# Kernel tuning notes

Measured on AMD Instinct MI355X. Metric: run time of the kernel, lower is better.

## Reference

```python
import jax, jax.numpy as jnp
import numpy as np

NUM_GROUPS = 32
EPS = 1e-5
HT_MIN = -1.0
HT_MAX = 1.0


def setup_inputs() -> dict:
    key = jax.random.key(0)
    k1, k2, k3 = jax.random.split(key, 3)
    B, IN, OUT = 8192, 2048, 4096
    x = jax.random.normal(k1, (B, IN), dtype=jnp.float32)
    # kaiming-uniform-ish scale for weight, uniform bias in [-1/sqrt(fan_in), 1/sqrt(fan_in)]
    bound_w = np.sqrt(1.0 / IN)
    weight = jax.random.uniform(k2, (OUT, IN), dtype=jnp.float32, minval=-bound_w, maxval=bound_w)
    bias = jax.random.uniform(k3, (OUT,), dtype=jnp.float32, minval=-bound_w, maxval=bound_w)
    return {"x": x, "weight": weight, "bias": bias}


def reference(x, weight, bias):
    # GEMM + bias: (B, out)
    y = jnp.einsum('bi,oi->bo', x, weight) + bias
    B, OUT = y.shape
    fpg = OUT // NUM_GROUPS
    g = y.reshape(B, NUM_GROUPS, fpg)
    mean = jnp.mean(g, axis=-1, keepdims=True)
    var = jnp.mean(jnp.square(g - mean), axis=-1, keepdims=True)  # biased variance
    x_hat = (g - mean) / jnp.sqrt(var + EPS)
    out = jnp.clip(x_hat, HT_MIN, HT_MAX)
    return out.reshape(B, OUT)
```

## Files before the change

kernel.cpp:

```cpp
#include <hip/hip_runtime.h>
#include <hip/hip_bf16.h>

#define B_ROWS   8192
#define K_DIM    2048
#define OUT_COLS 4096
#define EPS      1e-5f

#define BM 256
#define BN 256
#define BK 64
#define NT (K_DIM / BK)

using f32x4  = __attribute__((ext_vector_type(4))) float;
using bf16x8 = __attribute__((ext_vector_type(8))) short;

__device__ __forceinline__ unsigned short f2bf_rn(float f) {
    unsigned u = __builtin_bit_cast(unsigned, f);
    u += 0x7FFFu + ((u >> 16) & 1u);
    return (unsigned short)(u >> 16);
}

__global__ void cvt_bf16(const float* __restrict__ in, unsigned short* __restrict__ out, int n4) {
    int stride = gridDim.x * blockDim.x;
    for (int i = blockIdx.x * blockDim.x + threadIdx.x; i < n4; i += stride) {
        float4 v = reinterpret_cast<const float4*>(in)[i];
        ushort4 r;
        r.x = f2bf_rn(v.x); r.y = f2bf_rn(v.y); r.z = f2bf_rn(v.z); r.w = f2bf_rn(v.w);
        reinterpret_cast<ushort4*>(out)[i] = r;
    }
}

__device__ __forceinline__ void gload16(const unsigned short* src, unsigned short* lds) {
    __builtin_amdgcn_global_load_lds((const __attribute__((address_space(1))) void*)src,
                                     (__attribute__((address_space(3))) void*)lds,
                                     16, 0, 0);
}

#define STA(BUF, H, KT) do {                                                        \
    gload16(Ag + (H)*262144 + (KT)*64 + goff0, &As[BUF][(H)*8192 + lds0]);          \
    gload16(Ag + (H)*262144 + (KT)*64 + goff1, &As[BUF][(H)*8192 + lds1]);          \
  } while (0)
#define STB(BUF, H, KT) do {                                                        \
    gload16(Bg + (H)*262144 + (KT)*64 + goff0, &Bs[BUF][(H)*8192 + lds0]);          \
    gload16(Bg + (H)*262144 + (KT)*64 + goff1, &Bs[BUF][(H)*8192 + lds1]);          \
  } while (0)

#define RD_B(CURB) do {                                                             \
    _Pragma("unroll") for (int n = 0; n < 4; ++n) {                                 \
      const int ro = browb + n * 16 * BK;                                           \
      bb[n][0] = *(const bf16x8*)&(CURB)[ro + colsw0];                              \
      bb[n][1] = *(const bf16x8*)&(CURB)[ro + colsw1];                              \
    } } while (0)

#define RD_A(SLOT, CURA, Q) do {                                                    \
    _Pragma("unroll") for (int dm = 0; dm < 2; ++dm) {                              \
      const int ro = arow + (2*(Q)+dm) * 16 * BK;                                   \
      af[SLOT][dm][0] = *(const bf16x8*)&(CURA)[ro + colsw0];                       \
      af[SLOT][dm][1] = *(const bf16x8*)&(CURA)[ro + colsw1];                       \
    } } while (0)

#define MFMA16(SLOT, Q) do {                                                        \
    __builtin_amdgcn_s_setprio(1);                                                  \
    _Pragma("unroll") for (int kk = 0; kk < 2; ++kk)                                \
      _Pragma("unroll") for (int dm = 0; dm < 2; ++dm)                              \
        _Pragma("unroll") for (int n = 0; n < 4; ++n)                               \
          acc[2*(Q)+dm][n] = __builtin_amdgcn_mfma_f32_16x16x32_bf16(               \
              af[SLOT][dm][kk], bb[n][kk], acc[2*(Q)+dm][n], 0, 0, 0);              \
    __builtin_amdgcn_s_setprio(0);                                                  \
  } while (0)

#define VW4  asm volatile("s_waitcnt vmcnt(4)" ::: "memory")
#define BAR  __builtin_amdgcn_s_barrier()

__global__ __launch_bounds__(512, 2) void gemm_gn(const unsigned short* __restrict__ A,
                                                  const unsigned short* __restrict__ Bw,
                                                  const float* __restrict__ bias,
                                                  float* __restrict__ out) {
    __shared__ __align__(16) unsigned short As[2][BM * BK];
    __shared__ __align__(16) unsigned short Bs[2][BN * BK];

    const int tid  = threadIdx.x;
    const int lane = tid & 63;
    const int wave = tid >> 6;
    const int wr   = wave >> 2;
    const int wcn  = wave & 3;
    const int l16  = lane & 15;
    const int lhi  = lane >> 4;

    const int bid  = blockIdx.x;
    const int swz  = (bid & 7) * (gridDim.x >> 3) + (bid >> 3);
    const int brow = swz >> 4;
    const int bcol = swz & 15;

    int goff0, goff1, lds0, lds1;
    {
        int f0 = tid;          int r0 = f0 >> 3;
        int f1 = 512 + tid;    int r1 = f1 >> 3;
        goff0 = r0 * K_DIM + (((f0 & 7) ^ (r0 & 7)) * 8);
        goff1 = r1 * K_DIM + (((f1 & 7) ^ (r1 & 7)) * 8);
        lds0  = f0 * 8;
        lds1  = f1 * 8;
    }
    const unsigned short* Ag = A  + (size_t)brow * BM * K_DIM;
    const unsigned short* Bg = Bw + (size_t)bcol * BN * K_DIM;

    const int colsw0 = (0 * 32 + lhi * 8) ^ ((l16 & 7) << 3);
    const int colsw1 = (1 * 32 + lhi * 8) ^ ((l16 & 7) << 3);
    const int arow   = (wr * 128 + l16) * BK;
    const int browb  = (wcn * 64 + l16) * BK;

    const unsigned short* A0p = &As[0][0];
    const unsigned short* A1p = &As[1][0];
    const unsigned short* B0p = &Bs[0][0];
    const unsigned short* B1p = &Bs[1][0];

    f32x4  acc[8][4] = {};
    bf16x8 af[2][2][2];
    bf16x8 bb[4][2];

    STA(0, 0, 0); STA(0, 1, 0);
    STB(0, 0, 0); STB(0, 1, 0);
    STB(1, 0, 1); STB(1, 1, 1);
    VW4;
    BAR;
    RD_A(0, A0p, 0);
    RD_B(B0p);

    #pragma unroll 1
    for (int tt = 0; tt < NT; tt += 2) {
        const int k1 = (tt + 1) & (NT - 1);
        const int k2 = (tt + 2) & (NT - 1);
        const int k3 = (tt + 3) & (NT - 1);
        RD_A(1, A0p, 1); STA(1, 0, k1);               MFMA16(0, 0);       BAR;
        RD_A(0, A0p, 2); STA(1, 1, k1); STB(0, 0, k2); MFMA16(1, 1);      BAR;
        RD_A(1, A0p, 3); STB(0, 1, k2);               MFMA16(0, 2); VW4;  BAR;
        RD_A(0, A1p, 0);                              MFMA16(1, 3); RD_B(B1p); BAR;
        RD_A(1, A1p, 1); STA(0, 0, k2);               MFMA16(0, 0);       BAR;
        RD_A(0, A1p, 2); STA(0, 1, k2); STB(1, 0, k3); MFMA16(1, 1);      BAR;
        RD_A(1, A1p, 3); STB(1, 1, k3);               MFMA16(0, 2); VW4;  BAR;
        RD_A(0, A0p, 0);                              MFMA16(1, 3); RD_B(B0p); BAR;
    }

    asm volatile("s_waitcnt vmcnt(0)" ::: "memory");
    __syncthreads();
    float* red = (float*)&As[0][0];

    float bv[4];
    #pragma unroll
    for (int n = 0; n < 4; ++n)
        bv[n] = bias[bcol * BN + wcn * 64 + n * 16 + l16];

    #pragma unroll
    for (int m = 0; m < 8; ++m) {
        #pragma unroll
        for (int j = 0; j < 4; ++j) {
            float s = 0.f, s2 = 0.f;
            #pragma unroll
            for (int n = 0; n < 4; ++n) {
                float v = acc[m][n][j] + bv[n];
                acc[m][n][j] = v;
                s += v; s2 += v * v;
            }
            #pragma unroll
            for (int o = 1; o < 16; o <<= 1) {
                s  += __shfl_xor(s,  o);
                s2 += __shfl_xor(s2, o);
            }
            if (l16 == 0) {
                int r = wr * 128 + m * 16 + lhi * 4 + j;
                red[r * 8 + wcn * 2 + 0] = s;
                red[r * 8 + wcn * 2 + 1] = s2;
            }
        }
    }
    __syncthreads();

    const int p2 = (wcn & 2) * 2;
    #pragma unroll
    for (int m = 0; m < 8; ++m) {
        #pragma unroll
        for (int j = 0; j < 4; ++j) {
            const int r   = wr * 128 + m * 16 + lhi * 4 + j;
            const float s  = red[r * 8 + p2 + 0] + red[r * 8 + p2 + 2];
            const float s2 = red[r * 8 + p2 + 1] + red[r * 8 + p2 + 3];
            const float mean = s * (1.0f / 128.0f);
            const float var  = s2 * (1.0f / 128.0f) - mean * mean;
            const float rstd = rsqrtf(var + EPS);
            float* orow = out + (size_t)(brow * BM + r) * OUT_COLS + bcol * BN + wcn * 64 + l16;
            #pragma unroll
            for (int n = 0; n < 4; ++n) {
                float v = (acc[m][n][j] - mean) * rstd;
                v = fminf(fmaxf(v, -1.0f), 1.0f);
                orow[n * 16] = v;
            }
        }
    }
}

extern "C" void kernel_launch(void* const* d_in, const int* in_sizes, int n_in,
                              void* d_out, int out_size, void* d_ws, size_t ws_size,
                              hipStream_t stream) {
    const float* x    = (const float*)d_in[0];
    const float* w    = (const float*)d_in[1];
    const float* bias = (const float*)d_in[2];
    float* out        = (float*)d_out;

    unsigned short* xb = (unsigned short*)d_ws;
    unsigned short* wb = xb + (size_t)B_ROWS * K_DIM;

    cvt_bf16<<<2048, 256, 0, stream>>>(x, xb, (B_ROWS * K_DIM) / 4);
    cvt_bf16<<<1024, 256, 0, stream>>>(w, wb, (OUT_COLS * K_DIM) / 4);

    dim3 grid((B_ROWS / BM) * (OUT_COLS / BN));
    gemm_gn<<<grid, 512, 0, stream>>>(xb, wb, bias, out);
}
```

Measured before the change: 168.7 us.

## Switch GEMM to 32x32x16 MFMA with MFMA-native LDS layout and fuse conversions

Replaces the 16x16x32 bf16 MFMA tiling with 32x32x16 MFMA tiles, so each wave now holds 4x2 accumulators of 16 floats. The global-to-LDS staging is reorganized so each lane's fragment sits contiguously, replacing the XOR swizzle with a fragment-ordered layout. The epilogue row mapping is adapted to the 32x32 output layout. The two fp32-to-bf16 conversion kernels are merged into one launch. The aim is fewer MFMA issues and LDS reads per FLOP, at the risk of new LDS bank conflicts and higher register pressure.

```diff
diff --git a/kernel.cpp b/kernel.cpp
--- a/kernel.cpp
+++ b/kernel.cpp
@@ -11,7 +11,7 @@
 #define BK 64
 #define NT (K_DIM / BK)
 
-using f32x4  = __attribute__((ext_vector_type(4))) float;
+using f32x16 = __attribute__((ext_vector_type(16))) float;
 using bf16x8 = __attribute__((ext_vector_type(8))) short;
 
 __device__ __forceinline__ unsigned short f2bf_rn(float f) {
@@ -20,13 +20,19 @@
     return (unsigned short)(u >> 16);
 }
 
-__global__ void cvt_bf16(const float* __restrict__ in, unsigned short* __restrict__ out, int n4) {
+__global__ void cvt_all(const float* __restrict__ x, const float* __restrict__ w,
+                        unsigned short* __restrict__ xb, unsigned short* __restrict__ wb) {
+    const int n4x = (B_ROWS * K_DIM) / 4;
+    const int n4w = (OUT_COLS * K_DIM) / 4;
     int stride = gridDim.x * blockDim.x;
-    for (int i = blockIdx.x * blockDim.x + threadIdx.x; i < n4; i += stride) {
-        float4 v = reinterpret_cast<const float4*>(in)[i];
+    for (int i = blockIdx.x * blockDim.x + threadIdx.x; i < n4x + n4w; i += stride) {
+        const float4* src; ushort4* dst; int j;
+        if (i < n4x) { src = (const float4*)x; dst = (ushort4*)xb; j = i; }
+        else         { src = (const float4*)w; dst = (ushort4*)wb; j = i - n4x; }
+        float4 v = src[j];
         ushort4 r;
         r.x = f2bf_rn(v.x); r.y = f2bf_rn(v.y); r.z = f2bf_rn(v.z); r.w = f2bf_rn(v.w);
-        reinterpret_cast<ushort4*>(out)[i] = r;
+        dst[j] = r;
     }
 }
 
@@ -45,27 +51,23 @@
     gload16(Bg + (H)*262144 + (KT)*64 + goff1, &Bs[BUF][(H)*8192 + lds1]);          \
   } while (0)
 
-#define RD_B(CURB) do {                                                             \
-    _Pragma("unroll") for (int n = 0; n < 4; ++n) {                                 \
-      const int ro = browb + n * 16 * BK;                                           \
-      bb[n][0] = *(const bf16x8*)&(CURB)[ro + colsw0];                              \
-      bb[n][1] = *(const bf16x8*)&(CURB)[ro + colsw1];                              \
-    } } while (0)
-
-#define RD_A(SLOT, CURA, Q) do {                                                    \
-    _Pragma("unroll") for (int dm = 0; dm < 2; ++dm) {                              \
-      const int ro = arow + (2*(Q)+dm) * 16 * BK;                                   \
-      af[SLOT][dm][0] = *(const bf16x8*)&(CURA)[ro + colsw0];                       \
-      af[SLOT][dm][1] = *(const bf16x8*)&(CURA)[ro + colsw1];                       \
-    } } while (0)
-
-#define MFMA16(SLOT, Q) do {                                                        \
+#define RD_A(SLOT, BUFP, KS) do {                                                   \
+    _Pragma("unroll") for (int mt = 0; mt < 4; ++mt)                                \
+      af[SLOT][mt] = *(const bf16x8*)&(BUFP)[abase + mt*2048 + (KS)*512];           \
+  } while (0)
+
+#define RD_Bb(BUFP) do {                                                            \
+    _Pragma("unroll") for (int nt = 0; nt < 2; ++nt)                                \
+      _Pragma("unroll") for (int ks = 0; ks < 4; ++ks)                              \
+        bb[nt][ks] = *(const bf16x8*)&(BUFP)[bbase + nt*2048 + ks*512];             \
+  } while (0)
+
+#define MFMA8(SLOT, KS) do {                                                        \
     __builtin_amdgcn_s_setprio(1);                                                  \
-    _Pragma("unroll") for (int kk = 0; kk < 2; ++kk)                                \
-      _Pragma("unroll") for (int dm = 0; dm < 2; ++dm)                              \
-        _Pragma("unroll") for (int n = 0; n < 4; ++n)                               \
-          acc[2*(Q)+dm][n] = __builtin_amdgcn_mfma_f32_16x16x32_bf16(               \
-              af[SLOT][dm][kk], bb[n][kk], acc[2*(Q)+dm][n], 0, 0, 0);              \
+    _Pragma("unroll") for (int mt = 0; mt < 4; ++mt)                                \
+      _Pragma("unroll") for (int nt = 0; nt < 2; ++nt)                              \
+        acc[mt][nt] = __builtin_amdgcn_mfma_f32_32x32x16_bf16(                      \
+            af[SLOT][mt], bb[nt][KS], acc[mt][nt], 0, 0, 0);                        \
     __builtin_amdgcn_s_setprio(0);                                                  \
   } while (0)
 
@@ -76,16 +78,16 @@
                                                   const unsigned short* __restrict__ Bw,
                                                   const float* __restrict__ bias,
                                                   float* __restrict__ out) {
-    __shared__ __align__(16) unsigned short As[2][BM * BK];
-    __shared__ __align__(16) unsigned short Bs[2][BN * BK];
+    __shared__ __align__(16) unsigned short As[2][16384];
+    __shared__ __align__(16) unsigned short Bs[2][16384];
 
     const int tid  = threadIdx.x;
     const int lane = tid & 63;
     const int wave = tid >> 6;
     const int wr   = wave >> 2;
     const int wcn  = wave & 3;
-    const int l16  = lane & 15;
-    const int lhi  = lane >> 4;
+    const int l32  = lane & 31;
+    const int lhi  = lane >> 5;
 
     const int bid  = blockIdx.x;
     const int swz  = (bid & 7) * (gridDim.x >> 3) + (bid >> 3);
@@ -94,29 +96,26 @@
 
     int goff0, goff1, lds0, lds1;
     {
-        int f0 = tid;          int r0 = f0 >> 3;
-        int f1 = 512 + tid;    int r1 = f1 >> 3;
-        goff0 = r0 * K_DIM + (((f0 & 7) ^ (r0 & 7)) * 8);
-        goff1 = r1 * K_DIM + (((f1 & 7) ^ (r1 & 7)) * 8);
-        lds0  = f0 * 8;
-        lds1  = f1 * 8;
+        int s0 = tid, s1 = tid + 512;
+        goff0 = ((s0 >> 8) * 32 + (s0 & 31)) * K_DIM + ((s0 >> 6) & 3) * 16 + ((s0 >> 5) & 1) * 8;
+        goff1 = ((s1 >> 8) * 32 + (s1 & 31)) * K_DIM + ((s1 >> 6) & 3) * 16 + ((s1 >> 5) & 1) * 8;
+        lds0  = s0 * 8;
+        lds1  = s1 * 8;
     }
     const unsigned short* Ag = A  + (size_t)brow * BM * K_DIM;
     const unsigned short* Bg = Bw + (size_t)bcol * BN * K_DIM;
 
-    const int colsw0 = (0 * 32 + lhi * 8) ^ ((l16 & 7) << 3);
-    const int colsw1 = (1 * 32 + lhi * 8) ^ ((l16 & 7) << 3);
-    const int arow   = (wr * 128 + l16) * BK;
-    const int browb  = (wcn * 64 + l16) * BK;
+    const int abase = wr * 8192 + lane * 8;
+    const int bbase = (wcn >> 1) * 8192 + (wcn & 1) * 2 * 2048 + lane * 8;
 
     const unsigned short* A0p = &As[0][0];
     const unsigned short* A1p = &As[1][0];
     const unsigned short* B0p = &Bs[0][0];
     const unsigned short* B1p = &Bs[1][0];
 
-    f32x4  acc[8][4] = {};
-    bf16x8 af[2][2][2];
-    bf16x8 bb[4][2];
+    f32x16 acc[4][2] = {};
+    bf16x8 af[2][4];
+    bf16x8 bb[2][4];
 
     STA(0, 0, 0); STA(0, 1, 0);
     STB(0, 0, 0); STB(0, 1, 0);
@@ -124,50 +123,48 @@
     VW4;
     BAR;
     RD_A(0, A0p, 0);
-    RD_B(B0p);
+    RD_Bb(B0p);
 
     #pragma unroll 1
     for (int tt = 0; tt < NT; tt += 2) {
         const int k1 = (tt + 1) & (NT - 1);
         const int k2 = (tt + 2) & (NT - 1);
         const int k3 = (tt + 3) & (NT - 1);
-        RD_A(1, A0p, 1); STA(1, 0, k1);               MFMA16(0, 0);       BAR;
-        RD_A(0, A0p, 2); STA(1, 1, k1); STB(0, 0, k2); MFMA16(1, 1);      BAR;
-        RD_A(1, A0p, 3); STB(0, 1, k2);               MFMA16(0, 2); VW4;  BAR;
-        RD_A(0, A1p, 0);                              MFMA16(1, 3); RD_B(B1p); BAR;
-        RD_A(1, A1p, 1); STA(0, 0, k2);               MFMA16(0, 0);       BAR;
-        RD_A(0, A1p, 2); STA(0, 1, k2); STB(1, 0, k3); MFMA16(1, 1);      BAR;
-        RD_A(1, A1p, 3); STB(1, 1, k3);               MFMA16(0, 2); VW4;  BAR;
-        RD_A(0, A0p, 0);                              MFMA16(1, 3); RD_B(B0p); BAR;
+        RD_A(1, A0p, 1); STA(1, 0, k1);                MFMA8(0, 0);             BAR;
+        RD_A(0, A0p, 2); STA(1, 1, k1); STB(0, 0, k2); MFMA8(1, 1);             BAR;
+        RD_A(1, A0p, 3); STB(0, 1, k2);                MFMA8(0, 2); VW4;        BAR;
+        RD_A(0, A1p, 0);                               MFMA8(1, 3); RD_Bb(B1p); BAR;
+        RD_A(1, A1p, 1); STA(0, 0, k2);                MFMA8(0, 0);             BAR;
+        RD_A(0, A1p, 2); STA(0, 1, k2); STB(1, 0, k3); MFMA8(1, 1);             BAR;
+        RD_A(1, A1p, 3); STB(1, 1, k3);                MFMA8(0, 2); VW4;        BAR;
+        RD_A(0, A0p, 0);                               MFMA8(1, 3); RD_Bb(B0p); BAR;
     }
 
     asm volatile("s_waitcnt vmcnt(0)" ::: "memory");
     __syncthreads();
     float* red = (float*)&As[0][0];
 
-    float bv[4];
+    float bv[2];
     #pragma unroll
-    for (int n = 0; n < 4; ++n)
-        bv[n] = bias[bcol * BN + wcn * 64 + n * 16 + l16];
+    for (int nt = 0; nt < 2; ++nt)
+        bv[nt] = bias[bcol * BN + wcn * 64 + nt * 32 + l32];
 
     #pragma unroll
-    for (int m = 0; m < 8; ++m) {
+    for (int mt = 0; mt < 4; ++mt) {
         #pragma unroll
-        for (int j = 0; j < 4; ++j) {
-            float s = 0.f, s2 = 0.f;
+        for (int reg = 0; reg < 16; ++reg) {
+            float v0 = acc[mt][0][reg] + bv[0];
+            float v1 = acc[mt][1][reg] + bv[1];
+            acc[mt][0][reg] = v0;
+            acc[mt][1][reg] = v1;
+            float s = v0 + v1, s2 = v0 * v0 + v1 * v1;
             #pragma unroll
-            for (int n = 0; n < 4; ++n) {
-                float v = acc[m][n][j] + bv[n];
-                acc[m][n][j] = v;
-                s += v; s2 += v * v;
-            }
-            #pragma unroll
-            for (int o = 1; o < 16; o <<= 1) {
+            for (int o = 1; o < 32; o <<= 1) {
                 s  += __shfl_xor(s,  o);
                 s2 += __shfl_xor(s2, o);
             }
-            if (l16 == 0) {
-                int r = wr * 128 + m * 16 + lhi * 4 + j;
+            if (l32 == 0) {
+                int r = wr * 128 + mt * 32 + (reg & 3) + 8 * (reg >> 2) + 4 * lhi;
                 red[r * 8 + wcn * 2 + 0] = s;
                 red[r * 8 + wcn * 2 + 1] = s2;
             }
@@ -177,21 +174,21 @@
 
     const int p2 = (wcn & 2) * 2;
     #pragma unroll
-    for (int m = 0; m < 8; ++m) {
+    for (int mt = 0; mt < 4; ++mt) {
         #pragma unroll
-        for (int j = 0; j < 4; ++j) {
-            const int r   = wr * 128 + m * 16 + lhi * 4 + j;
+        for (int reg = 0; reg < 16; ++reg) {
+            const int r = wr * 128 + mt * 32 + (reg & 3) + 8 * (reg >> 2) + 4 * lhi;
             const float s  = red[r * 8 + p2 + 0] + red[r * 8 + p2 + 2];
             const float s2 = red[r * 8 + p2 + 1] + red[r * 8 + p2 + 3];
             const float mean = s * (1.0f / 128.0f);
             const float var  = s2 * (1.0f / 128.0f) - mean * mean;
             const float rstd = rsqrtf(var + EPS);
-            float* orow = out + (size_t)(brow * BM + r) * OUT_COLS + bcol * BN + wcn * 64 + l16;
+            float* orow = out + (size_t)(brow * BM + r) * OUT_COLS + bcol * BN + wcn * 64 + l32;
             #pragma unroll
-            for (int n = 0; n < 4; ++n) {
-                float v = (acc[m][n][j] - mean) * rstd;
+            for (int nt = 0; nt < 2; ++nt) {
+                float v = (acc[mt][nt][reg] - mean) * rstd;
                 v = fminf(fmaxf(v, -1.0f), 1.0f);
-                orow[n * 16] = v;
+                orow[nt * 32] = v;
             }
         }
     }
@@ -208,8 +205,7 @@
     unsigned short* xb = (unsigned short*)d_ws;
     unsigned short* wb = xb + (size_t)B_ROWS * K_DIM;
 
-    cvt_bf16<<<2048, 256, 0, stream>>>(x, xb, (B_ROWS * K_DIM) / 4);
-    cvt_bf16<<<1024, 256, 0, stream>>>(w, wb, (OUT_COLS * K_DIM) / 4);
+    cvt_all<<<3072, 256, 0, stream>>>(x, w, xb, wb);
 
     dim3 grid((B_ROWS / BM) * (OUT_COLS / BN));
     gemm_gn<<<grid, 512, 0, stream>>>(xb, wb, bias, out);
```

After: 242.5 us. 1.44x slower.

## Process two column tiles per block with prefetch across tiles and DPP reductions

Applied to the files above, without the earlier changes.

Each GEMM block now handles two 256-column output tiles in sequence, so the grid shrinks to 256 persistent-ish blocks. The next tile's first B and A stages are prefetched during the tail of the first tile's K loop. This hides the pipeline fill and the epilogue behind loads. Bias is folded into the accumulator init, and the shuffle reductions are replaced with DPP row adds. A separate reduction buffer is added in LDS. The two conversion kernels are merged into one launch. The change adds LDS usage and halves the block count, which may leave some CUs underused.

```diff
diff --git a/kernel.cpp b/kernel.cpp
--- a/kernel.cpp
+++ b/kernel.cpp
@@ -20,13 +20,19 @@
     return (unsigned short)(u >> 16);
 }
 
-__global__ void cvt_bf16(const float* __restrict__ in, unsigned short* __restrict__ out, int n4) {
+__global__ void cvt_all(const float* __restrict__ x, const float* __restrict__ w,
+                        unsigned short* __restrict__ xb, unsigned short* __restrict__ wb) {
+    const int n4x = (B_ROWS * K_DIM) / 4;
+    const int n4w = (OUT_COLS * K_DIM) / 4;
     int stride = gridDim.x * blockDim.x;
-    for (int i = blockIdx.x * blockDim.x + threadIdx.x; i < n4; i += stride) {
-        float4 v = reinterpret_cast<const float4*>(in)[i];
+    for (int i = blockIdx.x * blockDim.x + threadIdx.x; i < n4x + n4w; i += stride) {
+        const float4* src; ushort4* dst; int j;
+        if (i < n4x) { src = (const float4*)x; dst = (ushort4*)xb; j = i; }
+        else         { src = (const float4*)w; dst = (ushort4*)wb; j = i - n4x; }
+        float4 v = src[j];
         ushort4 r;
         r.x = f2bf_rn(v.x); r.y = f2bf_rn(v.y); r.z = f2bf_rn(v.z); r.w = f2bf_rn(v.w);
-        reinterpret_cast<ushort4*>(out)[i] = r;
+        dst[j] = r;
     }
 }
 
@@ -36,13 +42,26 @@
                                      16, 0, 0);
 }
 
-#define STA(BUF, H, KT) do {                                                        \
+__device__ __forceinline__ float rowsum16(float v) {
+    int x;
+    x = __builtin_amdgcn_update_dpp(0, __builtin_bit_cast(int, v), 0x121, 0xF, 0xF, true);
+    v += __builtin_bit_cast(float, x);
+    x = __builtin_amdgcn_update_dpp(0, __builtin_bit_cast(int, v), 0x122, 0xF, 0xF, true);
+    v += __builtin_bit_cast(float, x);
+    x = __builtin_amdgcn_update_dpp(0, __builtin_bit_cast(int, v), 0x124, 0xF, 0xF, true);
+    v += __builtin_bit_cast(float, x);
+    x = __builtin_amdgcn_update_dpp(0, __builtin_bit_cast(int, v), 0x128, 0xF, 0xF, true);
+    v += __builtin_bit_cast(float, x);
+    return v;
+}
+
+#define STA_(BUF, H, KT) do {                                                       \
     gload16(Ag + (H)*262144 + (KT)*64 + goff0, &As[BUF][(H)*8192 + lds0]);          \
     gload16(Ag + (H)*262144 + (KT)*64 + goff1, &As[BUF][(H)*8192 + lds1]);          \
   } while (0)
-#define STB(BUF, H, KT) do {                                                        \
-    gload16(Bg + (H)*262144 + (KT)*64 + goff0, &Bs[BUF][(H)*8192 + lds0]);          \
-    gload16(Bg + (H)*262144 + (KT)*64 + goff1, &Bs[BUF][(H)*8192 + lds1]);          \
+#define STB_(BASE, BUF, H, KT) do {                                                 \
+    gload16((BASE) + (H)*262144 + (KT)*64 + goff0, &Bs[BUF][(H)*8192 + lds0]);      \
+    gload16((BASE) + (H)*262144 + (KT)*64 + goff1, &Bs[BUF][(H)*8192 + lds1]);      \
   } while (0)
 
 #define RD_B(CURB) do {                                                             \
@@ -69,15 +88,64 @@
     __builtin_amdgcn_s_setprio(0);                                                  \
   } while (0)
 
-#define VW4  asm volatile("s_waitcnt vmcnt(4)" ::: "memory")
-#define BAR  __builtin_amdgcn_s_barrier()
+#define VW4   asm volatile("s_waitcnt vmcnt(4)" ::: "memory")
+#define VWALL asm volatile("s_waitcnt vmcnt(0)" ::: "memory")
+#define BAR   __builtin_amdgcn_s_barrier()
+
+#define ITER7(K1, B2B, K2, B3B, K3)                                                 \
+    RD_A(1, A0p, 1); STA_(1, 0, K1); STA_(1, 1, K1);           MFMA16(0, 0); BAR;   \
+    RD_A(0, A0p, 2); STB_(B2B, 0, 0, K2); STB_(B2B, 0, 1, K2); MFMA16(1, 1); BAR;   \
+    RD_A(1, A0p, 3);                                           MFMA16(0, 2); VW4; BAR; \
+    RD_A(0, A1p, 0);                                           MFMA16(1, 3); RD_B(B1p); BAR; \
+    RD_A(1, A1p, 1); STA_(0, 0, K2); STA_(0, 1, K2);           MFMA16(0, 0); BAR;   \
+    RD_A(0, A1p, 2); STB_(B3B, 1, 0, K3); STB_(B3B, 1, 1, K3); MFMA16(1, 1); BAR;   \
+    RD_A(1, A1p, 3);                                           MFMA16(0, 2); VW4; BAR;
+
+#define ACC_INIT(OCB) do {                                                          \
+    float bv[4];                                                                    \
+    _Pragma("unroll") for (int n = 0; n < 4; ++n)                                   \
+        bv[n] = bias[(OCB) + wcn * 64 + n * 16 + l16];                              \
+    _Pragma("unroll") for (int m = 0; m < 8; ++m)                                   \
+      _Pragma("unroll") for (int n = 0; n < 4; ++n)                                 \
+        _Pragma("unroll") for (int j = 0; j < 4; ++j)                               \
+            acc[m][n][j] = bv[n];                                                   \
+  } while (0)
+
+#define EPILOGUE(OCB) do {                                                          \
+    _Pragma("unroll") for (int m = 0; m < 8; ++m) {                                 \
+      _Pragma("unroll") for (int j = 0; j < 4; ++j) {                               \
+        float s = 0.f, s2 = 0.f;                                                    \
+        _Pragma("unroll") for (int n = 0; n < 4; ++n) {                             \
+            float v = acc[m][n][j]; s += v; s2 += v * v; }                          \
+        s = rowsum16(s); s2 = rowsum16(s2);                                         \
+        if (l16 == 0) {                                                             \
+            int r = wr * 128 + m * 16 + lhi * 4 + j;                                \
+            redbuf[r * 8 + wcn * 2 + 0] = s;                                        \
+            redbuf[r * 8 + wcn * 2 + 1] = s2;                                       \
+        } } }                                                                       \
+    __syncthreads();                                                                \
+    _Pragma("unroll") for (int m = 0; m < 8; ++m) {                                 \
+      _Pragma("unroll") for (int j = 0; j < 4; ++j) {                               \
+        const int r = wr * 128 + m * 16 + lhi * 4 + j;                              \
+        const float4 q = *(const float4*)&redbuf[r * 8 + p2];                       \
+        const float mean = (q.x + q.z) * (1.0f / 128.0f);                           \
+        const float var  = (q.y + q.w) * (1.0f / 128.0f) - mean * mean;             \
+        const float rstd = rsqrtf(var + EPS);                                       \
+        float* orow = out + (size_t)(brow * 256 + r) * OUT_COLS + (OCB) + wcn * 64 + l16; \
+        _Pragma("unroll") for (int n = 0; n < 4; ++n) {                             \
+            float v = (acc[m][n][j] - mean) * rstd;                                 \
+            v = fminf(fmaxf(v, -1.0f), 1.0f);                                       \
+            orow[n * 16] = v; } } }                                                 \
+    __syncthreads();                                                                \
+  } while (0)
 
 __global__ __launch_bounds__(512, 2) void gemm_gn(const unsigned short* __restrict__ A,
                                                   const unsigned short* __restrict__ Bw,
                                                   const float* __restrict__ bias,
                                                   float* __restrict__ out) {
-    __shared__ __align__(16) unsigned short As[2][BM * BK];
-    __shared__ __align__(16) unsigned short Bs[2][BN * BK];
+    __shared__ __align__(16) unsigned short As[2][16384];
+    __shared__ __align__(16) unsigned short Bs[2][16384];
+    __shared__ __align__(16) float redbuf[256 * 8];
 
     const int tid  = threadIdx.x;
     const int lane = tid & 63;
@@ -86,11 +154,12 @@
     const int wcn  = wave & 3;
     const int l16  = lane & 15;
     const int lhi  = lane >> 4;
+    const int p2   = (wcn & 2) * 2;
 
     const int bid  = blockIdx.x;
-    const int swz  = (bid & 7) * (gridDim.x >> 3) + (bid >> 3);
-    const int brow = swz >> 4;
-    const int bcol = swz & 15;
+    const int swz  = (bid & 7) * 32 + (bid >> 3);
+    const int brow = swz >> 3;
+    const int bc0  = swz & 7;
 
     int goff0, goff1, lds0, lds1;
     {
@@ -101,8 +170,11 @@
         lds0  = f0 * 8;
         lds1  = f1 * 8;
     }
-    const unsigned short* Ag = A  + (size_t)brow * BM * K_DIM;
-    const unsigned short* Bg = Bw + (size_t)bcol * BN * K_DIM;
+    const unsigned short* Ag  = A  + (size_t)brow * BM * K_DIM;
+    const unsigned short* Bg1 = Bw + (size_t)bc0 * BN * K_DIM;
+    const unsigned short* Bg2 = Bw + (size_t)(bc0 + 8) * BN * K_DIM;
+    const int ocb1 = bc0 * BN;
+    const int ocb2 = (bc0 + 8) * BN;
 
     const int colsw0 = (0 * 32 + lhi * 8) ^ ((l16 & 7) << 3);
     const int colsw1 = (1 * 32 + lhi * 8) ^ ((l16 & 7) << 3);
@@ -114,87 +186,49 @@
     const unsigned short* B0p = &Bs[0][0];
     const unsigned short* B1p = &Bs[1][0];
 
-    f32x4  acc[8][4] = {};
+    f32x4  acc[8][4];
     bf16x8 af[2][2][2];
     bf16x8 bb[4][2];
 
-    STA(0, 0, 0); STA(0, 1, 0);
-    STB(0, 0, 0); STB(0, 1, 0);
-    STB(1, 0, 1); STB(1, 1, 1);
+    ACC_INIT(ocb1);
+
+    STA_(0, 0, 0); STA_(0, 1, 0);
+    STB_(Bg1, 0, 0, 0); STB_(Bg1, 0, 1, 0);
+    STB_(Bg1, 1, 0, 1); STB_(Bg1, 1, 1, 1);
     VW4;
     BAR;
     RD_A(0, A0p, 0);
     RD_B(B0p);
 
     #pragma unroll 1
-    for (int tt = 0; tt < NT; tt += 2) {
-        const int k1 = (tt + 1) & (NT - 1);
-        const int k2 = (tt + 2) & (NT - 1);
-        const int k3 = (tt + 3) & (NT - 1);
-        RD_A(1, A0p, 1); STA(1, 0, k1);               MFMA16(0, 0);       BAR;
-        RD_A(0, A0p, 2); STA(1, 1, k1); STB(0, 0, k2); MFMA16(1, 1);      BAR;
-        RD_A(1, A0p, 3); STB(0, 1, k2);               MFMA16(0, 2); VW4;  BAR;
-        RD_A(0, A1p, 0);                              MFMA16(1, 3); RD_B(B1p); BAR;
-        RD_A(1, A1p, 1); STA(0, 0, k2);               MFMA16(0, 0);       BAR;
-        RD_A(0, A1p, 2); STA(0, 1, k2); STB(1, 0, k3); MFMA16(1, 1);      BAR;
-        RD_A(1, A1p, 3); STB(1, 1, k3);               MFMA16(0, 2); VW4;  BAR;
-        RD_A(0, A0p, 0);                              MFMA16(1, 3); RD_B(B0p); BAR;
-    }
-
-    asm volatile("s_waitcnt vmcnt(0)" ::: "memory");
-    __syncthreads();
-    float* red = (float*)&As[0][0];
-
-    float bv[4];
-    #pragma unroll
-    for (int n = 0; n < 4; ++n)
-        bv[n] = bias[bcol * BN + wcn * 64 + n * 16 + l16];
-
-    #pragma unroll
-    for (int m = 0; m < 8; ++m) {
-        #pragma unroll
-        for (int j = 0; j < 4; ++j) {
-            float s = 0.f, s2 = 0.f;
-            #pragma unroll
-            for (int n = 0; n < 4; ++n) {
-                float v = acc[m][n][j] + bv[n];
-                acc[m][n][j] = v;
-                s += v; s2 += v * v;
-            }
-            #pragma unroll
-            for (int o = 1; o < 16; o <<= 1) {
-                s  += __shfl_xor(s,  o);
-                s2 += __shfl_xor(s2, o);
-            }
-            if (l16 == 0) {
-                int r = wr * 128 + m * 16 + lhi * 4 + j;
-                red[r * 8 + wcn * 2 + 0] = s;
-                red[r * 8 + wcn * 2 + 1] = s2;
-            }
-        }
-    }
-    __syncthreads();
-
-    const int p2 = (wcn & 2) * 2;
-    #pragma unroll
-    for (int m = 0; m < 8; ++m) {
-        #pragma unroll
-        for (int j = 0; j < 4; ++j) {
-            const int r   = wr * 128 + m * 16 + lhi * 4 + j;
-            const float s  = red[r * 8 + p2 + 0] + red[r * 8 + p2 + 2];
-            const float s2 = red[r * 8 + p2 + 1] + red[r * 8 + p2 + 3];
-            const float mean = s * (1.0f / 128.0f);
-            const float var  = s2 * (1.0f / 128.0f) - mean * mean;
-            const float rstd = rsqrtf(var + EPS);
-            float* orow = out + (size_t)(brow * BM + r) * OUT_COLS + bcol * BN + wcn * 64 + l16;
-            #pragma unroll
-            for (int n = 0; n < 4; ++n) {
-                float v = (acc[m][n][j] - mean) * rstd;
-                v = fminf(fmaxf(v, -1.0f), 1.0f);
-                orow[n * 16] = v;
-            }
-        }
-    }
+    for (int tt = 0; tt < NT - 2; tt += 2) {
+        ITER7(tt + 1, Bg1, tt + 2, Bg1, tt + 3)
+        RD_A(0, A0p, 0); MFMA16(1, 3); RD_B(B0p); BAR;
+    }
+    ITER7(NT - 1, Bg2, 0, Bg2, 1)
+    MFMA16(1, 3); BAR;
+
+    EPILOGUE(ocb1);
+    ACC_INIT(ocb2);
+
+    RD_A(0, A0p, 0);
+    RD_B(B0p);
+
+    #pragma unroll 1
+    for (int tt = 0; tt < NT - 2; tt += 2) {
+        ITER7(tt + 1, Bg2, tt + 2, Bg2, tt + 3)
+        RD_A(0, A0p, 0); MFMA16(1, 3); RD_B(B0p); BAR;
+    }
+    RD_A(1, A0p, 1); STA_(1, 0, NT - 1); STA_(1, 1, NT - 1); MFMA16(0, 0); BAR;
+    RD_A(0, A0p, 2);                                         MFMA16(1, 1); BAR;
+    RD_A(1, A0p, 3);                                         MFMA16(0, 2); VWALL; BAR;
+    RD_A(0, A1p, 0);                                         MFMA16(1, 3); RD_B(B1p); BAR;
+    RD_A(1, A1p, 1);                                         MFMA16(0, 0); BAR;
+    RD_A(0, A1p, 2);                                         MFMA16(1, 1); BAR;
+    RD_A(1, A1p, 3);                                         MFMA16(0, 2); BAR;
+    MFMA16(1, 3);
+
+    EPILOGUE(ocb2);
 }
 
 extern "C" void kernel_launch(void* const* d_in, const int* in_sizes, int n_in,
@@ -208,9 +242,7 @@
     unsigned short* xb = (unsigned short*)d_ws;
     unsigned short* wb = xb + (size_t)B_ROWS * K_DIM;
 
-    cvt_bf16<<<2048, 256, 0, stream>>>(x, xb, (B_ROWS * K_DIM) / 4);
-    cvt_bf16<<<1024, 256, 0, stream>>>(w, wb, (OUT_COLS * K_DIM) / 4);
-
-    dim3 grid((B_ROWS / BM) * (OUT_COLS / BN));
-    gemm_gn<<<grid, 512, 0, stream>>>(xb, wb, bias, out);
-}
+    cvt_all<<<3072, 256, 0, stream>>>(x, w, xb, wb);
+
+    gemm_gn<<<256, 512, 0, stream>>>(xb, wb, bias, out);
+}
```

Measured after the change: 185.9 us. +10.2%, slower.
